# Kernel tuning notes

Hardware: AMD Instinct MI355X
Metric: run time of the kernel (lower is better)

The kernel has to match this reference:

```python
import jax, jax.numpy as jnp
import numpy as np

N, E, DIM = 50000, 1_600_000, 96
H = DIM // 3      # num_heads = dim/3 = 32
HD = 3            # head_dim = dim/num_heads = 3
SCALE = 2.0
EPS = 1e-5


def ln(x, g, b):
    mu = x.mean(-1, keepdims=True)
    var = ((x - mu) ** 2).mean(-1, keepdims=True)
    return (x - mu) * jax.lax.rsqrt(var + EPS) * g + b


def setup_inputs() -> dict:
    key = jax.random.key(0)
    ks = jax.random.split(key, 40)
    rn = lambda k, shp, s=0.05: jax.random.normal(k, shp, jnp.float32) * s
    inp = {
        'feat': jax.random.normal(ks[0], (N, DIM), jnp.float32),
        'edge': jax.random.normal(ks[1], (E, H), jnp.float32),
        'Wq': rn(ks[2], (DIM, DIM)), 'bq': jnp.zeros((DIM,), jnp.float32),
        'Wk': rn(ks[3], (DIM, DIM)), 'bk': jnp.zeros((DIM,), jnp.float32),
        'Wv': rn(ks[4], (DIM, DIM)), 'bv': jnp.zeros((DIM,), jnp.float32),
        'We': rn(ks[5], (H, H)), 'be': jnp.zeros((H,), jnp.float32),
        'Wb': rn(ks[6], (H, H)), 'bb': jnp.zeros((H,), jnp.float32),
        'Wvv': rn(ks[7], (DIM + H, DIM)), 'bvv': jnp.zeros((DIM,), jnp.float32),
        'Wf0': rn(ks[8], (H, 2 * H)), 'bf0': jnp.zeros((2 * H,), jnp.float32),
        'Wf1': rn(ks[9], (2 * H, H)), 'bf1': jnp.zeros((H,), jnp.float32),
        'Wm0': rn(ks[10], (DIM, 2 * DIM)), 'bm0': jnp.zeros((2 * DIM,), jnp.float32),
        'Wm1': rn(ks[11], (2 * DIM, DIM)), 'bm1': jnp.zeros((DIM,), jnp.float32),
        'g_n0': jnp.ones((DIM,), jnp.float32), 'b_n0': jnp.zeros((DIM,), jnp.float32),
        'g_e0': jnp.ones((H,), jnp.float32), 'b_e0': jnp.zeros((H,), jnp.float32),
        'g_e1': jnp.ones((H,), jnp.float32), 'b_e1': jnp.zeros((H,), jnp.float32),
        'g_m': jnp.ones((DIM,), jnp.float32), 'b_m': jnp.zeros((DIM,), jnp.float32),
        'w': jnp.zeros((1,), jnp.float32),
        'src': jax.random.randint(ks[12], (E,), 0, N),
        'dst': jax.random.randint(ks[13], (E,), 0, N),
    }
    return inp


def reference(feat, edge, Wq, bq, Wk, bk, Wv, bv, We, be, Wb, bb, Wvv, bvv,
              Wf0, bf0, Wf1, bf1, Wm0, bm0, Wm1, bm1,
              g_n0, b_n0, g_e0, b_e0, g_e1, b_e1, g_m, b_m, w, src, dst):
    n = feat.shape[0]
    h0 = ln(feat, g_n0, b_n0)            # [N, DIM]
    ew = ln(edge, g_e0, b_e0)            # [E, H]
    q = (h0 @ Wq + bq).reshape(n, H, HD)
    k = (h0 @ Wk + bk).reshape(n, H, HD)
    v = (h0 @ Wv + bv).reshape(n, H, HD)
    ve = (ew @ We + be)[:, :, None]       # [E, H, 1]
    B = ew @ Wb + bb                      # [E, H]
    # src_dot_dst('k','q'): (k[src] * q[dst]).sum(-1)
    score = jnp.sum(k[src] * q[dst], axis=-1) / SCALE + B   # [E, H]
    e = score + edge                       # [E, H]
    se = jnp.concatenate([v[src], ve], axis=-1)              # [E, H, 4]
    # edge_softmax: softmax over incoming edges of each dst node, per head
    m = jax.ops.segment_max(score, dst, num_segments=n)      # [N, H]
    ex = jnp.exp(score - m[dst])
    den = jax.ops.segment_sum(ex, dst, num_segments=n)
    att = (ex / den[dst])[:, :, None]                        # [E, H, 1]
    agg = jax.ops.segment_sum(att * se, dst, num_segments=n) # [N, H, 4]
    h = feat * (1.0 + w) + (agg.reshape(n, -1) @ Wvv + bvv)  # [N, DIM]
    # up_expert Mlp (pre-LN residual)
    hn = ln(h, g_m, b_m)
    h = h + (jax.nn.relu(hn @ Wm0 + bm0) @ Wm1 + bm1)
    # edge FFN residual
    en = ln(e, g_e1, b_e1)
    e = e + (jax.nn.relu(en @ Wf0 + bf0) @ Wf1 + bf1)
    return h, e
```

## Files before the change

### kernel.cpp

```cpp
#include <hip/hip_runtime.h>
#include <cstdint>
#include <cstddef>


typedef short  s16x8 __attribute__((ext_vector_type(8)));
typedef short  s16x4 __attribute__((ext_vector_type(4)));
typedef float  f32x4 __attribute__((ext_vector_type(4)));

__device__ __forceinline__ unsigned short f2b(float x) {
    union { float f; unsigned u; } v; v.f = x;
    unsigned r = v.u + 0x7FFF + ((v.u >> 16) & 1);
    return (unsigned short)(r >> 16);
}
__device__ __forceinline__ float b2f(unsigned short u) {
    union { unsigned u; float f; } v; v.u = ((unsigned)u) << 16; return v.f;
}

template<int MULTI, int LNA, int A16, int RELU, int RES>
__global__ __launch_bounds__(256) void mgemm_kernel(
    const void* __restrict__ Av, int lda,
    const float* __restrict__ B0, const float* __restrict__ B1,
    const float* __restrict__ B2, int ldb,
    const float* __restrict__ bias0, const float* __restrict__ bias1,
    const float* __restrict__ bias2,
    const float* __restrict__ lng, const float* __restrict__ lnbv,
    const float* __restrict__ resid, const float* __restrict__ wptr,
    float* __restrict__ C, int ldc, unsigned short* __restrict__ C16,
    int M, int K)
{
    __shared__ unsigned short sAL[64 * 200];
    __shared__ unsigned short sB[96 * 40];

    const int tid = threadIdx.x;
    const int m0 = blockIdx.x * 64;
    const int y  = blockIdx.y;
    const float* B = MULTI ? (y == 0 ? B0 : (y == 1 ? B1 : B2)) : B0;
    const int nbB = MULTI ? 0 : y * 96;
    const int nbC = y * 96;
    const int w = tid >> 6, l = tid & 63, fr = l & 15, kg = l >> 4;
    const int KP = K + 8;

    if (LNA) {
        const float* Af = (const float*)Av;
        const int row = 16 * w + fr;
        const int grow = m0 + row;
        float x[24];
        if (grow < M) {
            #pragma unroll
            for (int t = 0; t < 6; t++)
                *(float4*)&x[t * 4] = *(const float4*)(Af + (size_t)grow * lda + 24 * kg + t * 4);
        } else {
            #pragma unroll
            for (int t = 0; t < 24; t++) x[t] = 0.f;
        }
        float s = 0.f;
        #pragma unroll
        for (int t = 0; t < 24; t++) s += x[t];
        s += __shfl_xor(s, 16, 64); s += __shfl_xor(s, 32, 64);
        float mu = s * (1.f / 96.f);
        float v2 = 0.f;
        #pragma unroll
        for (int t = 0; t < 24; t++) { float d = x[t] - mu; v2 += d * d; }
        v2 += __shfl_xor(v2, 16, 64); v2 += __shfl_xor(v2, 32, 64);
        float rs = rsqrtf(v2 * (1.f / 96.f) + 1e-5f);
        #pragma unroll
        for (int t3 = 0; t3 < 3; t3++) {
            s16x8 yv;
            #pragma unroll
            for (int u = 0; u < 8; u++) {
                int cidx = 24 * kg + t3 * 8 + u;
                yv[u] = (short)f2b((x[t3 * 8 + u] - mu) * rs * lng[cidx] + lnbv[cidx]);
            }
            *(s16x8*)&sAL[row * KP + 24 * kg + t3 * 8] = yv;
        }
    } else {
        const int nseg = K >> 3;
        for (int idx = tid; idx < 64 * nseg; idx += 256) {
            int row = idx / nseg, k8 = (idx - row * nseg) * 8;
            int grow = m0 + row;
            s16x8 a8 = (s16x8){0, 0, 0, 0, 0, 0, 0, 0};
            if (grow < M) {
                if (A16) {
                    a8 = *(const s16x8*)((const unsigned short*)Av + (size_t)grow * lda + k8);
                } else {
                    const float* Af = (const float*)Av;
                    float4 v0 = *(const float4*)(Af + (size_t)grow * lda + k8);
                    float4 v1 = *(const float4*)(Af + (size_t)grow * lda + k8 + 4);
                    a8[0] = (short)f2b(v0.x); a8[1] = (short)f2b(v0.y);
                    a8[2] = (short)f2b(v0.z); a8[3] = (short)f2b(v0.w);
                    a8[4] = (short)f2b(v1.x); a8[5] = (short)f2b(v1.y);
                    a8[6] = (short)f2b(v1.z); a8[7] = (short)f2b(v1.w);
                }
            }
            *(s16x8*)&sAL[row * KP + k8] = a8;
        }
    }

    f32x4 acc[6];
    #pragma unroll
    for (int i = 0; i < 6; i++) acc[i] = (f32x4){0.f, 0.f, 0.f, 0.f};

    for (int kc = 0; kc < K; kc += 32) {
        #pragma unroll
        for (int r = 0; r < 3; r++) {
            int idx = tid + 256 * r;
            int k = idx / 24, n4 = (idx - k * 24) * 4;
            float4 v = *(const float4*)(B + (size_t)(kc + k) * ldb + nbB + n4);
            sB[(n4 + 0) * 40 + k] = f2b(v.x);
            sB[(n4 + 1) * 40 + k] = f2b(v.y);
            sB[(n4 + 2) * 40 + k] = f2b(v.z);
            sB[(n4 + 3) * 40 + k] = f2b(v.w);
        }
        __syncthreads();
        {
            s16x8 a = *(s16x8*)&sAL[(16 * w + fr) * KP + kc + kg * 8];
            #pragma unroll
            for (int nt = 0; nt < 6; nt++) {
                s16x8 b = *(s16x8*)&sB[(16 * nt + fr) * 40 + kg * 8];
                acc[nt] = __builtin_amdgcn_mfma_f32_16x16x32_bf16(a, b, acc[nt], 0, 0, 0);
            }
        }
        __syncthreads();
    }

    float scale = 1.f;
    if (RES) scale = wptr ? (1.f + wptr[0]) : 1.f;
    const float* biasp = MULTI ? (y == 0 ? bias0 : (y == 1 ? bias1 : bias2)) : bias0;
    const int bbase = MULTI ? 0 : nbB;

    #pragma unroll
    for (int nt = 0; nt < 6; nt++) {
        int cl = nt * 16 + fr;
        float bv = biasp[bbase + cl];
        int gcol = nbC + cl;
        #pragma unroll
        for (int r = 0; r < 4; r++) {
            int row = m0 + 16 * w + 4 * kg + r;
            if (row >= M) continue;
            float v = acc[nt][r] + bv;
            if (RELU) v = fmaxf(v, 0.f);
            if (MULTI) {
                C16[(size_t)row * 288 + gcol] = f2b(v);
            } else {
                if (RES) v += scale * resid[(size_t)row * ldc + gcol];
                C[(size_t)row * ldc + gcol] = v;
            }
        }
    }
}

__global__ __launch_bounds__(256) void count_kernel(
    const int* __restrict__ dst, int* __restrict__ cnt,
    int* __restrict__ rank, int E)
{
    int i = blockIdx.x * 256 + threadIdx.x;
    if (i < E) rank[i] = atomicAdd(&cnt[dst[i]], 1);
}

__global__ __launch_bounds__(1024) void scan_kernel(
    const int* __restrict__ cnt, int* __restrict__ off, int N)
{
    __shared__ int s[1024];
    const int tid = threadIdx.x;
    const int chunk = (N + 1023) >> 10;
    const int lo = tid * chunk;
    const int hi = min(lo + chunk, N);
    int sum = 0;
    for (int i = lo; i < hi; i++) sum += cnt[i];
    s[tid] = sum;
    __syncthreads();
    for (int d = 1; d < 1024; d <<= 1) {
        int v = (tid >= d) ? s[tid - d] : 0;
        __syncthreads();
        s[tid] += v;
        __syncthreads();
    }
    int base = (tid == 0) ? 0 : s[tid - 1];
    for (int i = lo; i < hi; i++) {
        off[i] = base;
        base += cnt[i];
    }
}

__global__ __launch_bounds__(256) void scatter_kernel(
    const int* __restrict__ dst, const int* __restrict__ src,
    const int* __restrict__ off, const int* __restrict__ rank,
    int* __restrict__ eidx, int* __restrict__ srcs, int* __restrict__ dsts, int E)
{
    int i = blockIdx.x * 256 + threadIdx.x;
    if (i < E) {
        int p = off[dst[i]] + rank[i];
        eidx[p] = i;
        srcs[p] = src[i];
        dsts[p] = dst[i];
    }
}

__global__ __launch_bounds__(256, 4) void edge_tile_kernel(
    const float* __restrict__ edge, const unsigned short* __restrict__ qkv16,
    const int* __restrict__ eidx, const int* __restrict__ srcs,
    const int* __restrict__ dsts,
    const float* __restrict__ We, const float* __restrict__ be,
    const float* __restrict__ Wb, const float* __restrict__ bb,
    const float* __restrict__ Wf0, const float* __restrict__ bf0,
    const float* __restrict__ Wf1, const float* __restrict__ bf1,
    const float* __restrict__ ge0, const float* __restrict__ be0,
    const float* __restrict__ ge1, const float* __restrict__ be1,
    unsigned short* __restrict__ exve16, float* __restrict__ eout, int E)
{
    __shared__ float          sEV[64 * 36];
    __shared__ unsigned short sQK[64 * 44];
    __shared__ unsigned short sA [64 * 40];
    __shared__ unsigned short sB [64 * 40];
    __shared__ unsigned short sB2[32 * 72];
    __shared__ unsigned short sX [64 * 76];

    const int tid = threadIdx.x;
    const long long e0 = (long long)blockIdx.x * 64;
    const int w  = tid >> 6;
    const int l  = tid & 63;
    const int fr = l & 15;
    const int kg = l >> 4;

    {
        const int row = tid >> 2;
        const int j   = tid & 3;
        long long s = e0 + row;
        float qv[24], kv[24];
        if (s < E) {
            int dn = dsts[s], sn = srcs[s];
            const unsigned short* qp = qkv16 + (size_t)dn * 288 + 24 * j;
            const unsigned short* kp = qkv16 + (size_t)sn * 288 + 96 + 24 * j;
            #pragma unroll
            for (int t = 0; t < 3; t++) {
                s16x8 qa = *(const s16x8*)(qp + 8 * t);
                s16x8 ka = *(const s16x8*)(kp + 8 * t);
                #pragma unroll
                for (int u = 0; u < 8; u++) {
                    qv[8 * t + u] = b2f((unsigned short)qa[u]);
                    kv[8 * t + u] = b2f((unsigned short)ka[u]);
                }
            }
        } else {
            #pragma unroll
            for (int t = 0; t < 24; t++) { qv[t] = 0.f; kv[t] = 0.f; }
        }
        s16x8 qkb;
        #pragma unroll
        for (int t = 0; t < 8; t++) {
            float d = kv[3*t]*qv[3*t] + kv[3*t+1]*qv[3*t+1] + kv[3*t+2]*qv[3*t+2];
            qkb[t] = (short)f2b(0.5f * d);
        }
        *(s16x8*)&sQK[row * 44 + 8 * j] = qkb;
    }

    #pragma unroll
    for (int rr = 0; rr < 2; rr++) {
        int idx = tid + 256 * rr;
        int row = idx >> 3, c4 = (idx & 7) * 4;
        long long s = e0 + row;
        float4 v = make_float4(0.f, 0.f, 0.f, 0.f);
        if (s < E) {
            int ge = eidx[s];
            v = *(const float4*)(edge + (size_t)ge * 32 + c4);
        }
        *(float4*)&sEV[row * 36 + c4] = v;
    }
    {
        int k = tid >> 3, c4 = (tid & 7) * 4;
        float4 vb = *(const float4*)(Wb + k * 32 + c4);
        float4 ve = *(const float4*)(We + k * 32 + c4);
        sB[(c4 + 0) * 40 + k] = f2b(vb.x); sB[(c4 + 1) * 40 + k] = f2b(vb.y);
        sB[(c4 + 2) * 40 + k] = f2b(vb.z); sB[(c4 + 3) * 40 + k] = f2b(vb.w);
        sB[(32 + c4 + 0) * 40 + k] = f2b(ve.x); sB[(32 + c4 + 1) * 40 + k] = f2b(ve.y);
        sB[(32 + c4 + 2) * 40 + k] = f2b(ve.z); sB[(32 + c4 + 3) * 40 + k] = f2b(ve.w);
    }
    #pragma unroll
    for (int rr = 0; rr < 2; rr++) {
        int idx = tid + 256 * rr;
        int k = idx >> 3, c4 = (idx & 7) * 4;
        float4 v = *(const float4*)(Wf1 + k * 32 + c4);
        sB2[(c4 + 0) * 72 + k] = f2b(v.x); sB2[(c4 + 1) * 72 + k] = f2b(v.y);
        sB2[(c4 + 2) * 72 + k] = f2b(v.z); sB2[(c4 + 3) * 72 + k] = f2b(v.w);
    }
    __syncthreads();

    {
        const int row = 16 * w + (tid & 15);
        const int q = (tid & 63) >> 4;
        float x[8];
        *(float4*)&x[0] = *(float4*)&sEV[row * 36 + 8 * q];
        *(float4*)&x[4] = *(float4*)&sEV[row * 36 + 8 * q + 4];
        float s = x[0] + x[1] + x[2] + x[3] + x[4] + x[5] + x[6] + x[7];
        s += __shfl_xor(s, 16, 64); s += __shfl_xor(s, 32, 64);
        float mu = s * (1.f / 32.f);
        float v2 = 0.f;
        #pragma unroll
        for (int i = 0; i < 8; i++) { float d = x[i] - mu; v2 += d * d; }
        v2 += __shfl_xor(v2, 16, 64); v2 += __shfl_xor(v2, 32, 64);
        float rs = rsqrtf(v2 * (1.f / 32.f) + 1e-5f);
        float4 g1 = *(const float4*)(ge0 + 8 * q), g2 = *(const float4*)(ge0 + 8 * q + 4);
        float4 b1 = *(const float4*)(be0 + 8 * q), b2 = *(const float4*)(be0 + 8 * q + 4);
        float gg[8] = {g1.x, g1.y, g1.z, g1.w, g2.x, g2.y, g2.z, g2.w};
        float bs[8] = {b1.x, b1.y, b1.z, b1.w, b2.x, b2.y, b2.z, b2.w};
        s16x8 y;
        #pragma unroll
        for (int i = 0; i < 8; i++)
            y[i] = (short)f2b((x[i] - mu) * rs * gg[i] + bs[i]);
        *(s16x8*)&sA[row * 40 + 8 * q] = y;
    }
    __syncthreads();

    f32x4 acc[4];
    {
        s16x8 a = *(s16x8*)&sA[(16 * w + fr) * 40 + kg * 8];
        #pragma unroll
        for (int nt = 0; nt < 4; nt++) {
            s16x8 b = *(s16x8*)&sB[(16 * nt + fr) * 40 + kg * 8];
            f32x4 z = {0.f, 0.f, 0.f, 0.f};
            acc[nt] = __builtin_amdgcn_mfma_f32_16x16x32_bf16(a, b, z, 0, 0, 0);
        }
    }
    __syncthreads();

    #pragma unroll
    for (int nt = 0; nt < 2; nt++) {
        int col = nt * 16 + fr;
        float bbv = bb[col];
        #pragma unroll
        for (int r = 0; r < 4; r++) {
            int row = 16 * w + 4 * kg + r;
            float sc = acc[nt][r] + b2f(sQK[row * 44 + col]) + bbv;
            sX[row * 76 + col] = f2b(__expf(sc));
            float er = sc + sEV[row * 36 + col];
            sEV[row * 36 + col] = er;
        }
    }
    #pragma unroll
    for (int nt = 2; nt < 4; nt++) {
        int col = (nt - 2) * 16 + fr;
        float bev = be[col];
        #pragma unroll
        for (int r = 0; r < 4; r++) {
            int row = 16 * w + 4 * kg + r;
            sX[row * 76 + 32 + col] = f2b(acc[nt][r] + bev);
        }
    }
    #pragma unroll
    for (int rr = 0; rr < 2; rr++) {
        int idx = tid + 256 * rr;
        int k = idx >> 4, c4 = (idx & 15) * 4;
        float4 v = *(const float4*)(Wf0 + k * 64 + c4);
        sB[(c4 + 0) * 40 + k] = f2b(v.x); sB[(c4 + 1) * 40 + k] = f2b(v.y);
        sB[(c4 + 2) * 40 + k] = f2b(v.z); sB[(c4 + 3) * 40 + k] = f2b(v.w);
    }
    __syncthreads();

    #pragma unroll
    for (int rr = 0; rr < 2; rr++) {
        int idx = tid + 256 * rr;
        int row = idx >> 3, c8 = (idx & 7) * 8;
        long long s = e0 + row;
        if (s < E)
            *(s16x8*)(exve16 + (size_t)s * 64 + c8) = *(s16x8*)&sX[row * 76 + c8];
    }
    {
        const int row = 16 * w + (tid & 15);
        const int q = (tid & 63) >> 4;
        float x[8];
        *(float4*)&x[0] = *(float4*)&sEV[row * 36 + 8 * q];
        *(float4*)&x[4] = *(float4*)&sEV[row * 36 + 8 * q + 4];
        float s = x[0] + x[1] + x[2] + x[3] + x[4] + x[5] + x[6] + x[7];
        s += __shfl_xor(s, 16, 64); s += __shfl_xor(s, 32, 64);
        float mu = s * (1.f / 32.f);
        float v2 = 0.f;
        #pragma unroll
        for (int i = 0; i < 8; i++) { float d = x[i] - mu; v2 += d * d; }
        v2 += __shfl_xor(v2, 16, 64); v2 += __shfl_xor(v2, 32, 64);
        float rs = rsqrtf(v2 * (1.f / 32.f) + 1e-5f);
        float4 g1 = *(const float4*)(ge1 + 8 * q), g2 = *(const float4*)(ge1 + 8 * q + 4);
        float4 b1 = *(const float4*)(be1 + 8 * q), b2 = *(const float4*)(be1 + 8 * q + 4);
        float gg[8] = {g1.x, g1.y, g1.z, g1.w, g2.x, g2.y, g2.z, g2.w};
        float bs[8] = {b1.x, b1.y, b1.z, b1.w, b2.x, b2.y, b2.z, b2.w};
        s16x8 y;
        #pragma unroll
        for (int i = 0; i < 8; i++)
            y[i] = (short)f2b((x[i] - mu) * rs * gg[i] + bs[i]);
        *(s16x8*)&sA[row * 40 + 8 * q] = y;
    }
    __syncthreads();

    {
        s16x8 a = *(s16x8*)&sA[(16 * w + fr) * 40 + kg * 8];
        #pragma unroll
        for (int nt = 0; nt < 4; nt++) {
            s16x8 b = *(s16x8*)&sB[(16 * nt + fr) * 40 + kg * 8];
            f32x4 z = {0.f, 0.f, 0.f, 0.f};
            f32x4 a2 = __builtin_amdgcn_mfma_f32_16x16x32_bf16(a, b, z, 0, 0, 0);
            int col = nt * 16 + fr;
            float b0v = bf0[col];
            #pragma unroll
            for (int r = 0; r < 4; r++) {
                int row = 16 * w + 4 * kg + r;
                sX[row * 76 + col] = f2b(fmaxf(a2[r] + b0v, 0.f));
            }
        }
    }
    __syncthreads();

    {
        s16x8 a0 = *(s16x8*)&sX[(16 * w + fr) * 76 + kg * 8];
        s16x8 a1 = *(s16x8*)&sX[(16 * w + fr) * 76 + 32 + kg * 8];
        #pragma unroll
        for (int nt = 0; nt < 2; nt++) {
            s16x8 b0 = *(s16x8*)&sB2[(16 * nt + fr) * 72 + kg * 8];
            s16x8 b1 = *(s16x8*)&sB2[(16 * nt + fr) * 72 + 32 + kg * 8];
            f32x4 z = {0.f, 0.f, 0.f, 0.f};
            f32x4 t = __builtin_amdgcn_mfma_f32_16x16x32_bf16(a0, b0, z, 0, 0, 0);
            t = __builtin_amdgcn_mfma_f32_16x16x32_bf16(a1, b1, t, 0, 0, 0);
            int col = nt * 16 + fr;
            float bf1v = bf1[col];
            #pragma unroll
            for (int r = 0; r < 4; r++) {
                int row = 16 * w + 4 * kg + r;
                float out = t[r] + sEV[row * 36 + col] + bf1v;
                sEV[row * 36 + col] = out;
            }
        }
    }
    __syncthreads();

    #pragma unroll
    for (int rr = 0; rr < 2; rr++) {
        int idx = tid + 256 * rr;
        int row = idx >> 3, c4 = (idx & 7) * 4;
        long long s = e0 + row;
        if (s < E) {
            int ge = eidx[s];
            *(float4*)(eout + (size_t)ge * 32 + c4) = *(float4*)&sEV[row * 36 + c4];
        }
    }
}

__global__ __launch_bounds__(256) void gather_kernel(
    const unsigned short* __restrict__ exve16, const unsigned short* __restrict__ qkv16,
    const int* __restrict__ srcs, const int* __restrict__ off,
    const int* __restrict__ cnt, unsigned short* __restrict__ agg16, int N)
{
    __shared__ unsigned short sV16[4][2][2][96];
    __shared__ unsigned short sE16[4][2][2][64];
    const int wave = threadIdx.x >> 6;
    const int lane = threadIdx.x & 63;
    const int head = lane & 31;
    const int half = lane >> 5;
    int n = blockIdx.x * 4 + wave;
    if (n >= N) return;
    const int o = off[n], d = cnt[n];
    float a0 = 0.f, a1 = 0.f, a2 = 0.f, a3 = 0.f, den = 0.f;
    for (int i = half; i < d; i += 4) {
        const int i2 = i + 2;
        {
            int sn = srcs[o + i];
            const unsigned short* vr = qkv16 + (size_t)sn * 288 + 192;
            const unsigned short* er = exve16 + (size_t)(o + i) * 64;
            if (head < 12)
                *(s16x8*)&sV16[wave][half][0][head * 8] = *(const s16x8*)(vr + head * 8);
            else if (head >= 24)
                *(s16x8*)&sE16[wave][half][0][(head - 24) * 8] = *(const s16x8*)(er + (head - 24) * 8);
        }
        if (i2 < d) {
            int sn = srcs[o + i2];
            const unsigned short* vr = qkv16 + (size_t)sn * 288 + 192;
            const unsigned short* er = exve16 + (size_t)(o + i2) * 64;
            if (head < 12)
                *(s16x8*)&sV16[wave][half][1][head * 8] = *(const s16x8*)(vr + head * 8);
            else if (head >= 24)
                *(s16x8*)&sE16[wave][half][1][(head - 24) * 8] = *(const s16x8*)(er + (head - 24) * 8);
        }
        __builtin_amdgcn_wave_barrier();
        {
            float ex = b2f(sE16[wave][half][0][head]);
            float vv = b2f(sE16[wave][half][0][32 + head]);
            a0 += ex * b2f(sV16[wave][half][0][head * 3]);
            a1 += ex * b2f(sV16[wave][half][0][head * 3 + 1]);
            a2 += ex * b2f(sV16[wave][half][0][head * 3 + 2]);
            a3 += ex * vv;
            den += ex;
        }
        if (i2 < d) {
            float ex = b2f(sE16[wave][half][1][head]);
            float vv = b2f(sE16[wave][half][1][32 + head]);
            a0 += ex * b2f(sV16[wave][half][1][head * 3]);
            a1 += ex * b2f(sV16[wave][half][1][head * 3 + 1]);
            a2 += ex * b2f(sV16[wave][half][1][head * 3 + 2]);
            a3 += ex * vv;
            den += ex;
        }
        __builtin_amdgcn_wave_barrier();
    }
    a0 += __shfl_xor(a0, 32, 64);
    a1 += __shfl_xor(a1, 32, 64);
    a2 += __shfl_xor(a2, 32, 64);
    a3 += __shfl_xor(a3, 32, 64);
    den += __shfl_xor(den, 32, 64);
    if (half == 0) {
        float sc = (d > 0) ? 1.f / den : 0.f;
        s16x4 ov;
        ov[0] = (short)f2b(a0 * sc);
        ov[1] = (short)f2b(a1 * sc);
        ov[2] = (short)f2b(a2 * sc);
        ov[3] = (short)f2b(a3 * sc);
        *(s16x4*)(agg16 + (size_t)n * 128 + head * 4) = ov;
    }
}

extern "C" void kernel_launch(void* const* d_in, const int* in_sizes, int n_in,
                              void* d_out, int out_size, void* d_ws, size_t ws_size,
                              hipStream_t stream)
{
    (void)n_in; (void)out_size; (void)ws_size;
    const float* feat = (const float*)d_in[0];
    const float* edge = (const float*)d_in[1];
    const float* Wq   = (const float*)d_in[2];
    const float* bq   = (const float*)d_in[3];
    const float* Wk   = (const float*)d_in[4];
    const float* bk   = (const float*)d_in[5];
    const float* Wv   = (const float*)d_in[6];
    const float* bv   = (const float*)d_in[7];
    const float* We   = (const float*)d_in[8];
    const float* be   = (const float*)d_in[9];
    const float* Wb   = (const float*)d_in[10];
    const float* bb   = (const float*)d_in[11];
    const float* Wvv  = (const float*)d_in[12];
    const float* bvv  = (const float*)d_in[13];
    const float* Wf0  = (const float*)d_in[14];
    const float* bf0  = (const float*)d_in[15];
    const float* Wf1  = (const float*)d_in[16];
    const float* bf1  = (const float*)d_in[17];
    const float* Wm0  = (const float*)d_in[18];
    const float* bm0  = (const float*)d_in[19];
    const float* Wm1  = (const float*)d_in[20];
    const float* bm1  = (const float*)d_in[21];
    const float* g_n0 = (const float*)d_in[22];
    const float* b_n0 = (const float*)d_in[23];
    const float* g_e0 = (const float*)d_in[24];
    const float* b_e0 = (const float*)d_in[25];
    const float* g_e1 = (const float*)d_in[26];
    const float* b_e1 = (const float*)d_in[27];
    const float* g_m  = (const float*)d_in[28];
    const float* b_m  = (const float*)d_in[29];
    const float* wsc  = (const float*)d_in[30];
    const int*   src  = (const int*)d_in[31];
    const int*   dst  = (const int*)d_in[32];

    const int N = in_sizes[0] / 96;
    const int E = in_sizes[1] / 32;

    float* ws    = (float*)d_ws;
    float* hp    = ws;
    float* tbuf  = hp + (size_t)N * 96;
    unsigned short* agg16 = (unsigned short*)(tbuf + (size_t)N * 192);
    unsigned short* qkv16 = agg16 + (size_t)N * 128;
    unsigned short* exve16 = qkv16 + (size_t)N * 288;
    int*   eidx  = (int*)(exve16 + (size_t)E * 64);
    int*   rank  = eidx + E;
    int*   srcs  = rank + E;
    int*   dsts  = srcs + E;
    int*   cnt   = dsts + E;
    int*   offv  = cnt + N;
    float* hout  = (float*)d_out;
    float* eoutp = (float*)d_out + (size_t)N * 96;

    hipMemsetAsync(cnt, 0, (size_t)N * sizeof(int), stream);

    const int mt = (N + 63) / 64;
    const int et = (E + 255) / 256;

    count_kernel<<<et, 256, 0, stream>>>(dst, cnt, rank, E);
    scan_kernel<<<1, 1024, 0, stream>>>(cnt, offv, N);
    scatter_kernel<<<et, 256, 0, stream>>>(dst, src, offv, rank, eidx, srcs, dsts, E);

    mgemm_kernel<1,1,0,0,0><<<dim3(mt, 3), 256, 0, stream>>>(
        feat, 96, Wq, Wk, Wv, 96, bq, bk, bv, g_n0, b_n0,
        nullptr, nullptr, nullptr, 0, qkv16, N, 96);

    edge_tile_kernel<<<(E + 63) / 64, 256, 0, stream>>>(edge, qkv16, eidx, srcs, dsts,
                                             We, be, Wb, bb, Wf0, bf0, Wf1, bf1,
                                             g_e0, b_e0, g_e1, b_e1,
                                             exve16, eoutp, E);

    gather_kernel<<<(N + 3) / 4, 256, 0, stream>>>(exve16, qkv16, srcs, offv, cnt, agg16, N);

    mgemm_kernel<0,0,1,0,1><<<dim3(mt, 1), 256, 0, stream>>>(
        agg16, 128, Wvv, Wvv, Wvv, 96, bvv, bvv, bvv, nullptr, nullptr,
        feat, wsc, hp, 96, nullptr, N, 128);
    mgemm_kernel<0,1,0,1,0><<<dim3(mt, 2), 256, 0, stream>>>(
        hp, 96, Wm0, Wm0, Wm0, 192, bm0, bm0, bm0, g_m, b_m,
        nullptr, nullptr, tbuf, 192, nullptr, N, 96);
    mgemm_kernel<0,0,0,0,1><<<dim3(mt, 1), 256, 0, stream>>>(
        tbuf, 192, Wm1, Wm1, Wm1, 96, bm1, bm1, bm1, nullptr, nullptr,
        hp, nullptr, hout, 96, nullptr, N, 192);
}
```

Baseline: 826.8 us.

## Precompute transposed bf16 edge weights once and read MFMA operands from global

A new one-block prep kernel converts Wb/We, Wf0 and Wf1 to transposed bf16 layouts once per call. The edge tile kernel then loads MFMA B operands straight from global/L2 instead of staging each weight matrix into shared memory in every block. This removes per-block weight conversion and stores and frees LDS, which permits a higher occupancy hint (5 blocks). It also replaces several block-wide barriers with wave barriers where each wave only touches its own rows. The cost is extra global/cache loads per MFMA and one more kernel launch.

```diff
diff --git a/kernel.cpp b/kernel.cpp
--- a/kernel.cpp
+++ b/kernel.cpp
@@ -149,6 +149,28 @@
     }
 }
 
+__global__ __launch_bounds__(256) void prep_kernel(
+    const float* __restrict__ Wb, const float* __restrict__ We,
+    const float* __restrict__ Wf0, const float* __restrict__ Wf1,
+    unsigned short* __restrict__ WbWe16, unsigned short* __restrict__ Wf0T16,
+    unsigned short* __restrict__ Wf1T16)
+{
+    const int t = threadIdx.x;
+    for (int i = t; i < 2048; i += 256) {
+        int n = i >> 5, k = i & 31;
+        float v = (n < 32) ? Wb[k * 32 + n] : We[k * 32 + (n - 32)];
+        WbWe16[i] = f2b(v);
+    }
+    for (int i = t; i < 2048; i += 256) {
+        int n = i >> 5, k = i & 31;
+        Wf0T16[i] = f2b(Wf0[k * 64 + n]);
+    }
+    for (int i = t; i < 2048; i += 256) {
+        int n = i >> 6, k = i & 63;
+        Wf1T16[i] = f2b(Wf1[k * 32 + n]);
+    }
+}
+
 __global__ __launch_bounds__(256) void count_kernel(
     const int* __restrict__ dst, int* __restrict__ cnt,
     int* __restrict__ rank, int E)
@@ -196,14 +218,15 @@
     }
 }
 
-__global__ __launch_bounds__(256, 4) void edge_tile_kernel(
+__global__ __launch_bounds__(256, 5) void edge_tile_kernel(
     const float* __restrict__ edge, const unsigned short* __restrict__ qkv16,
     const int* __restrict__ eidx, const int* __restrict__ srcs,
     const int* __restrict__ dsts,
-    const float* __restrict__ We, const float* __restrict__ be,
-    const float* __restrict__ Wb, const float* __restrict__ bb,
-    const float* __restrict__ Wf0, const float* __restrict__ bf0,
-    const float* __restrict__ Wf1, const float* __restrict__ bf1,
+    const unsigned short* __restrict__ WbWe16,
+    const unsigned short* __restrict__ Wf0T16,
+    const unsigned short* __restrict__ Wf1T16,
+    const float* __restrict__ be, const float* __restrict__ bb,
+    const float* __restrict__ bf0, const float* __restrict__ bf1,
     const float* __restrict__ ge0, const float* __restrict__ be0,
     const float* __restrict__ ge1, const float* __restrict__ be1,
     unsigned short* __restrict__ exve16, float* __restrict__ eout, int E)
@@ -211,8 +234,6 @@
     __shared__ float          sEV[64 * 36];
     __shared__ unsigned short sQK[64 * 44];
     __shared__ unsigned short sA [64 * 40];
-    __shared__ unsigned short sB [64 * 40];
-    __shared__ unsigned short sB2[32 * 72];
     __shared__ unsigned short sX [64 * 76];
 
     const int tid = threadIdx.x;
@@ -253,7 +274,6 @@
         }
         *(s16x8*)&sQK[row * 44 + 8 * j] = qkb;
     }
-
     #pragma unroll
     for (int rr = 0; rr < 2; rr++) {
         int idx = tid + 256 * rr;
@@ -265,23 +285,6 @@
             v = *(const float4*)(edge + (size_t)ge * 32 + c4);
         }
         *(float4*)&sEV[row * 36 + c4] = v;
-    }
-    {
-        int k = tid >> 3, c4 = (tid & 7) * 4;
-        float4 vb = *(const float4*)(Wb + k * 32 + c4);
-        float4 ve = *(const float4*)(We + k * 32 + c4);
-        sB[(c4 + 0) * 40 + k] = f2b(vb.x); sB[(c4 + 1) * 40 + k] = f2b(vb.y);
-        sB[(c4 + 2) * 40 + k] = f2b(vb.z); sB[(c4 + 3) * 40 + k] = f2b(vb.w);
-        sB[(32 + c4 + 0) * 40 + k] = f2b(ve.x); sB[(32 + c4 + 1) * 40 + k] = f2b(ve.y);
-        sB[(32 + c4 + 2) * 40 + k] = f2b(ve.z); sB[(32 + c4 + 3) * 40 + k] = f2b(ve.w);
-    }
-    #pragma unroll
-    for (int rr = 0; rr < 2; rr++) {
-        int idx = tid + 256 * rr;
-        int k = idx >> 3, c4 = (idx & 7) * 4;
-        float4 v = *(const float4*)(Wf1 + k * 32 + c4);
-        sB2[(c4 + 0) * 72 + k] = f2b(v.x); sB2[(c4 + 1) * 72 + k] = f2b(v.y);
-        sB2[(c4 + 2) * 72 + k] = f2b(v.z); sB2[(c4 + 3) * 72 + k] = f2b(v.w);
     }
     __syncthreads();
 
@@ -309,19 +312,18 @@
             y[i] = (short)f2b((x[i] - mu) * rs * gg[i] + bs[i]);
         *(s16x8*)&sA[row * 40 + 8 * q] = y;
     }
-    __syncthreads();
+    __builtin_amdgcn_wave_barrier();
 
     f32x4 acc[4];
     {
         s16x8 a = *(s16x8*)&sA[(16 * w + fr) * 40 + kg * 8];
         #pragma unroll
         for (int nt = 0; nt < 4; nt++) {
-            s16x8 b = *(s16x8*)&sB[(16 * nt + fr) * 40 + kg * 8];
+            s16x8 b = *(const s16x8*)(WbWe16 + (16 * nt + fr) * 32 + kg * 8);
             f32x4 z = {0.f, 0.f, 0.f, 0.f};
             acc[nt] = __builtin_amdgcn_mfma_f32_16x16x32_bf16(a, b, z, 0, 0, 0);
         }
     }
-    __syncthreads();
 
     #pragma unroll
     for (int nt = 0; nt < 2; nt++) {
@@ -345,14 +347,6 @@
             int row = 16 * w + 4 * kg + r;
             sX[row * 76 + 32 + col] = f2b(acc[nt][r] + bev);
         }
-    }
-    #pragma unroll
-    for (int rr = 0; rr < 2; rr++) {
-        int idx = tid + 256 * rr;
-        int k = idx >> 4, c4 = (idx & 15) * 4;
-        float4 v = *(const float4*)(Wf0 + k * 64 + c4);
-        sB[(c4 + 0) * 40 + k] = f2b(v.x); sB[(c4 + 1) * 40 + k] = f2b(v.y);
-        sB[(c4 + 2) * 40 + k] = f2b(v.z); sB[(c4 + 3) * 40 + k] = f2b(v.w);
     }
     __syncthreads();
 
@@ -394,7 +388,7 @@
         s16x8 a = *(s16x8*)&sA[(16 * w + fr) * 40 + kg * 8];
         #pragma unroll
         for (int nt = 0; nt < 4; nt++) {
-            s16x8 b = *(s16x8*)&sB[(16 * nt + fr) * 40 + kg * 8];
+            s16x8 b = *(const s16x8*)(Wf0T16 + (16 * nt + fr) * 32 + kg * 8);
             f32x4 z = {0.f, 0.f, 0.f, 0.f};
             f32x4 a2 = __builtin_amdgcn_mfma_f32_16x16x32_bf16(a, b, z, 0, 0, 0);
             int col = nt * 16 + fr;
@@ -406,15 +400,15 @@
             }
         }
     }
-    __syncthreads();
+    __builtin_amdgcn_wave_barrier();
 
     {
         s16x8 a0 = *(s16x8*)&sX[(16 * w + fr) * 76 + kg * 8];
         s16x8 a1 = *(s16x8*)&sX[(16 * w + fr) * 76 + 32 + kg * 8];
         #pragma unroll
         for (int nt = 0; nt < 2; nt++) {
-            s16x8 b0 = *(s16x8*)&sB2[(16 * nt + fr) * 72 + kg * 8];
-            s16x8 b1 = *(s16x8*)&sB2[(16 * nt + fr) * 72 + 32 + kg * 8];
+            s16x8 b0 = *(const s16x8*)(Wf1T16 + (16 * nt + fr) * 64 + kg * 8);
+            s16x8 b1 = *(const s16x8*)(Wf1T16 + (16 * nt + fr) * 64 + 32 + kg * 8);
             f32x4 z = {0.f, 0.f, 0.f, 0.f};
             f32x4 t = __builtin_amdgcn_mfma_f32_16x16x32_bf16(a0, b0, z, 0, 0, 0);
             t = __builtin_amdgcn_mfma_f32_16x16x32_bf16(a1, b1, t, 0, 0, 0);
@@ -562,7 +556,10 @@
     unsigned short* agg16 = (unsigned short*)(tbuf + (size_t)N * 192);
     unsigned short* qkv16 = agg16 + (size_t)N * 128;
     unsigned short* exve16 = qkv16 + (size_t)N * 288;
-    int*   eidx  = (int*)(exve16 + (size_t)E * 64);
+    unsigned short* wbwe16 = exve16 + (size_t)E * 64;
+    unsigned short* wf0t16 = wbwe16 + 2048;
+    unsigned short* wf1t16 = wf0t16 + 2048;
+    int*   eidx  = (int*)(wf1t16 + 2048);
     int*   rank  = eidx + E;
     int*   srcs  = rank + E;
     int*   dsts  = srcs + E;
@@ -576,6 +573,7 @@
     const int mt = (N + 63) / 64;
     const int et = (E + 255) / 256;
 
+    prep_kernel<<<1, 256, 0, stream>>>(Wb, We, Wf0, Wf1, wbwe16, wf0t16, wf1t16);
     count_kernel<<<et, 256, 0, stream>>>(dst, cnt, rank, E);
     scan_kernel<<<1, 1024, 0, stream>>>(cnt, offv, N);
     scatter_kernel<<<et, 256, 0, stream>>>(dst, src, offv, rank, eidx, srcs, dsts, E);
@@ -585,7 +583,8 @@
         nullptr, nullptr, nullptr, 0, qkv16, N, 96);
 
     edge_tile_kernel<<<(E + 63) / 64, 256, 0, stream>>>(edge, qkv16, eidx, srcs, dsts,
-                                             We, be, Wb, bb, Wf0, bf0, Wf1, bf1,
+                                             wbwe16, wf0t16, wf1t16,
+                                             be, bb, bf0, bf1,
                                              g_e0, b_e0, g_e1, b_e1,
                                              exve16, eoutp, E);
 
```

After: 818.8 us. No clear change (-1.0%).
